# Optimization experiments

Hardware: AMD Instinct MI355X
Metric: run time of the kernel (lower is better)

The kernel has to match this reference:

```python
import jax, jax.numpy as jnp
import numpy as np

B, L1, L2, H = 16, 1024, 1024, 768

def setup_inputs() -> dict:
    key = jax.random.key(0)
    k1, k2, k3, k4, k5, k6 = jax.random.split(key, 6)
    x1 = jax.random.normal(k1, (B, L1, H), dtype=jnp.float32)
    x2 = jax.random.normal(k2, (B, L2, H), dtype=jnp.float32)
    # True = padded position (masked out), matching torch masked_fill_ semantics
    x1_mask = jax.random.randint(k3, (B, L1), 0, 2) == 1
    x2_mask = jax.random.randint(k4, (B, L2), 0, 2) == 1
    # shared nn.Linear(H, H) used for both x and y projections
    W = jax.random.normal(k5, (H, H), dtype=jnp.float32) / np.sqrt(H)
    b = jax.random.normal(k6, (H,), dtype=jnp.float32) * 0.01
    return {"x1": x1, "x2": x2, "x1_mask": x1_mask, "x2_mask": x2_mask, "W": W, "b": b}

def reference(x1, x2, x1_mask, x2_mask, W, b):
    # SeqAttnMatch('relu_FC', normalize='sumY') with z = y = x2
    x_proj = jax.nn.relu(jnp.einsum('bid,hd->bih', x1, W) + b)   # [B,L1,H]
    y_proj = jax.nn.relu(jnp.einsum('bjd,hd->bjh', x2, W) + b)   # [B,L2,H]
    scores = jnp.einsum('bih,bjh->bij', x_proj, y_proj)          # [B,L1,L2]
    scores = jnp.where(x2_mask[:, None, :], -jnp.inf, scores)
    alpha = jax.nn.softmax(scores, axis=-1)                      # sum over len2
    att = jnp.einsum('bij,bjd->bid', alpha, x2)                  # [B,L1,H]
    # inter_att_concat = 'concat_dot_diff'
    return jnp.concatenate([x1, att, x1 * att, x1 - att], axis=2)  # [B,L1,4H]
```

## Files before the change

### kernel.cpp

```cpp
#include <hip/hip_runtime.h>


#define B_  16
#define L_  1024
#define H_  768
#define M1_ (B_ * L_)
#define MT_ (2 * M1_)

using f32x4  = __attribute__((ext_vector_type(4))) float;
using bf16x8 = __attribute__((ext_vector_type(8))) __bf16;
using u16x8  = __attribute__((ext_vector_type(8))) unsigned short;
using u16x4  = __attribute__((ext_vector_type(4))) unsigned short;

__device__ inline unsigned short f2b(float f) {
  unsigned u = __builtin_bit_cast(unsigned, f);
  u += 0x7FFFu + ((u >> 16) & 1u);
  return (unsigned short)(u >> 16);
}
__device__ inline float b2f(unsigned short u) {
  return __builtin_bit_cast(float, ((unsigned)u) << 16);
}

__device__ inline bf16x8 ld_frag(const unsigned short* lds, int row, int quad) {
  u16x8 v = *(const u16x8*)(lds + row * 40 + quad * 8);
  return __builtin_bit_cast(bf16x8, v);
}

#define MFMA(a, b, c) __builtin_amdgcn_mfma_f32_16x16x32_bf16((a), (b), (c), 0, 0, 0)

__global__ __launch_bounds__(256) void k_proj(
    const float* __restrict__ x1, const float* __restrict__ x2,
    const float* __restrict__ W, const float* __restrict__ bias,
    unsigned short* __restrict__ Ph, unsigned short* __restrict__ Pl)
{
  __shared__ unsigned short Ah[128 * 40];
  __shared__ unsigned short Al[128 * 40];
  __shared__ unsigned short Bh[128 * 40];
  __shared__ unsigned short Bl[128 * 40];

  const int tid  = threadIdx.x;
  const int lane = tid & 63, wv = tid >> 6;
  const int wr = wv >> 1, wc = wv & 1;
  const int quad = lane >> 4, lx = lane & 15;

  const int n0 = blockIdx.x * 128;
  const int m0 = blockIdx.y * 128;
  const float* Xb = (m0 < M1_) ? (x1 + (size_t)m0 * H_)
                               : (x2 + (size_t)(m0 - M1_) * H_);

  const int srow = tid >> 1;
  const int scol = (tid & 1) * 16;

  f32x4 acc[4][4] = {};

  for (int k0 = 0; k0 < H_; k0 += 32) {
    __syncthreads();
    const float* sa = Xb + (size_t)srow * H_ + k0 + scol;
    const float* sb = W + (size_t)(n0 + srow) * H_ + k0 + scol;
#pragma unroll
    for (int c = 0; c < 16; c += 4) {
      f32x4 va = *(const f32x4*)(sa + c);
      f32x4 vb = *(const f32x4*)(sb + c);
      u16x4 ha, la, hb, lb;
#pragma unroll
      for (int q = 0; q < 4; ++q) {
        ha[q] = f2b(va[q]); la[q] = f2b(va[q] - b2f(ha[q]));
        hb[q] = f2b(vb[q]); lb[q] = f2b(vb[q] - b2f(hb[q]));
      }
      *(u16x4*)(Ah + srow * 40 + scol + c) = ha;
      *(u16x4*)(Al + srow * 40 + scol + c) = la;
      *(u16x4*)(Bh + srow * 40 + scol + c) = hb;
      *(u16x4*)(Bl + srow * 40 + scol + c) = lb;
    }
    __syncthreads();

    bf16x8 fah[4], fal[4], fbh[4], fbl[4];
#pragma unroll
    for (int t = 0; t < 4; ++t) {
      fah[t] = ld_frag(Ah, wr * 64 + t * 16 + lx, quad);
      fal[t] = ld_frag(Al, wr * 64 + t * 16 + lx, quad);
      fbh[t] = ld_frag(Bh, wc * 64 + t * 16 + lx, quad);
      fbl[t] = ld_frag(Bl, wc * 64 + t * 16 + lx, quad);
    }
#pragma unroll
    for (int i = 0; i < 4; ++i)
#pragma unroll
      for (int j = 0; j < 4; ++j) {
        acc[i][j] = MFMA(fah[i], fbh[j], acc[i][j]);
        acc[i][j] = MFMA(fah[i], fbl[j], acc[i][j]);
        acc[i][j] = MFMA(fal[i], fbh[j], acc[i][j]);
      }
  }

#pragma unroll
  for (int j = 0; j < 4; ++j) {
    const int h = n0 + wc * 64 + j * 16 + lx;
    const float bv = bias[h];
#pragma unroll
    for (int i = 0; i < 4; ++i) {
      const int mb = m0 + wr * 64 + i * 16 + quad * 4;
#pragma unroll
      for (int r = 0; r < 4; ++r) {
        float v = acc[i][j][r] + bv;
        v = v > 0.f ? v : 0.f;
        const unsigned short hh = f2b(v);
        const unsigned short ll = f2b(v - b2f(hh));
        const size_t off = (size_t)(mb + r) * H_ + h;
        Ph[off] = hh;
        Pl[off] = ll;
      }
    }
  }
}

__global__ __launch_bounds__(256) void k_scores(
    const unsigned short* __restrict__ Ph, const unsigned short* __restrict__ Pl,
    const int* __restrict__ x2_mask, float* __restrict__ scores)
{
  __shared__ unsigned short Ah[128 * 40];
  __shared__ unsigned short Al[128 * 40];
  __shared__ unsigned short Bh[128 * 40];
  __shared__ unsigned short Bl[128 * 40];

  const int tid  = threadIdx.x;
  const int lane = tid & 63, wv = tid >> 6;
  const int wr = wv >> 1, wc = wv & 1;
  const int quad = lane >> 4, lx = lane & 15;

  const int j0 = blockIdx.x * 128;
  const int i0 = blockIdx.y * 128;
  const int b  = blockIdx.z;

  const size_t arow = (size_t)(b * L_ + i0);
  const size_t brow = (size_t)(M1_ + b * L_ + j0);

  const int srow = tid >> 1;
  const int scol = (tid & 1) * 16;

  f32x4 acc[4][4] = {};

  for (int k0 = 0; k0 < H_; k0 += 32) {
    __syncthreads();
    const size_t aoff = (arow + srow) * H_ + k0 + scol;
    const size_t boff = (brow + srow) * H_ + k0 + scol;
#pragma unroll
    for (int c = 0; c < 16; c += 8) {
      *(u16x8*)(Ah + srow * 40 + scol + c) = *(const u16x8*)(Ph + aoff + c);
      *(u16x8*)(Al + srow * 40 + scol + c) = *(const u16x8*)(Pl + aoff + c);
      *(u16x8*)(Bh + srow * 40 + scol + c) = *(const u16x8*)(Ph + boff + c);
      *(u16x8*)(Bl + srow * 40 + scol + c) = *(const u16x8*)(Pl + boff + c);
    }
    __syncthreads();

    bf16x8 fah[4], fal[4], fbh[4], fbl[4];
#pragma unroll
    for (int t = 0; t < 4; ++t) {
      fah[t] = ld_frag(Ah, wr * 64 + t * 16 + lx, quad);
      fal[t] = ld_frag(Al, wr * 64 + t * 16 + lx, quad);
      fbh[t] = ld_frag(Bh, wc * 64 + t * 16 + lx, quad);
      fbl[t] = ld_frag(Bl, wc * 64 + t * 16 + lx, quad);
    }
#pragma unroll
    for (int i = 0; i < 4; ++i)
#pragma unroll
      for (int j = 0; j < 4; ++j) {
        acc[i][j] = MFMA(fah[i], fbh[j], acc[i][j]);
        acc[i][j] = MFMA(fah[i], fbl[j], acc[i][j]);
        acc[i][j] = MFMA(fal[i], fbh[j], acc[i][j]);
      }
  }

#pragma unroll
  for (int j = 0; j < 4; ++j) {
    const int jj = j0 + wc * 64 + j * 16 + lx;
    const int mv = x2_mask[b * L_ + jj];
#pragma unroll
    for (int i = 0; i < 4; ++i) {
      const int ib = i0 + wr * 64 + i * 16 + quad * 4;
#pragma unroll
      for (int r = 0; r < 4; ++r) {
        const float v = mv ? -1e30f : acc[i][j][r];
        scores[((size_t)(b * L_) + ib + r) * L_ + jj] = v;
      }
    }
  }
}

__global__ __launch_bounds__(256) void k_softmax(float* __restrict__ scores)
{
  const size_t row = blockIdx.x;
  float* p = scores + row * L_;
  const int tid = threadIdx.x;

  f32x4 v = *(const f32x4*)(p + tid * 4);
  float m = fmaxf(fmaxf(v[0], v[1]), fmaxf(v[2], v[3]));
#pragma unroll
  for (int off = 32; off > 0; off >>= 1) m = fmaxf(m, __shfl_down(m, off));

  __shared__ float rmax[4];
  __shared__ float rsum[4];
  const int wid = tid >> 6, lane = tid & 63;
  if (lane == 0) rmax[wid] = m;
  __syncthreads();
  m = fmaxf(fmaxf(rmax[0], rmax[1]), fmaxf(rmax[2], rmax[3]));

  f32x4 e;
#pragma unroll
  for (int q = 0; q < 4; ++q) e[q] = __expf(v[q] - m);
  float s = e[0] + e[1] + e[2] + e[3];
#pragma unroll
  for (int off = 32; off > 0; off >>= 1) s += __shfl_down(s, off);
  if (lane == 0) rsum[wid] = s;
  __syncthreads();
  s = rsum[0] + rsum[1] + rsum[2] + rsum[3];

  const float inv = 1.0f / s;
#pragma unroll
  for (int q = 0; q < 4; ++q) e[q] *= inv;
  *(f32x4*)(p + tid * 4) = e;
}

__global__ __launch_bounds__(256) void k_att(
    const float* __restrict__ alpha, const float* __restrict__ x2,
    float* __restrict__ att)
{
  __shared__ unsigned short Aa[128 * 40];
  __shared__ unsigned short Bt[128 * 40];

  const int tid  = threadIdx.x;
  const int lane = tid & 63, wv = tid >> 6;
  const int wr = wv >> 1, wc = wv & 1;
  const int quad = lane >> 4, lx = lane & 15;

  const int d0 = blockIdx.x * 128;
  const int i0 = blockIdx.y * 128;
  const int b  = blockIdx.z;

  const int srow = tid >> 1;
  const int scol = (tid & 1) * 16;

  f32x4 acc[4][4] = {};

  for (int j0 = 0; j0 < L_; j0 += 32) {
    __syncthreads();
    const float* sa = alpha + ((size_t)(b * L_) + i0 + srow) * L_ + j0 + scol;
#pragma unroll
    for (int c = 0; c < 16; c += 4) {
      f32x4 va = *(const f32x4*)(sa + c);
      u16x4 h;
#pragma unroll
      for (int q = 0; q < 4; ++q) h[q] = f2b(va[q]);
      *(u16x4*)(Aa + srow * 40 + scol + c) = h;
    }
#pragma unroll
    for (int pp = 0; pp < 4; ++pp) {
      const int idx = tid + pp * 256;
      const int jj  = idx >> 5;
      const int dd  = (idx & 31) * 4;
      f32x4 vb = *(const f32x4*)(x2 + ((size_t)(b * L_) + j0 + jj) * H_ + d0 + dd);
#pragma unroll
      for (int q = 0; q < 4; ++q) Bt[(dd + q) * 40 + jj] = f2b(vb[q]);
    }
    __syncthreads();

    bf16x8 fa[4], fb[4];
#pragma unroll
    for (int t = 0; t < 4; ++t) {
      fa[t] = ld_frag(Aa, wr * 64 + t * 16 + lx, quad);
      fb[t] = ld_frag(Bt, wc * 64 + t * 16 + lx, quad);
    }
#pragma unroll
    for (int i = 0; i < 4; ++i)
#pragma unroll
      for (int j = 0; j < 4; ++j)
        acc[i][j] = MFMA(fa[i], fb[j], acc[i][j]);
  }

#pragma unroll
  for (int j = 0; j < 4; ++j) {
    const int dd = d0 + wc * 64 + j * 16 + lx;
#pragma unroll
    for (int i = 0; i < 4; ++i) {
      const int ib = i0 + wr * 64 + i * 16 + quad * 4;
#pragma unroll
      for (int r = 0; r < 4; ++r)
        att[((size_t)(b * L_) + ib + r) * H_ + dd] = acc[i][j][r];
    }
  }
}

__global__ __launch_bounds__(256) void k_concat(
    const float* __restrict__ x1, const float* __restrict__ att,
    float* __restrict__ out)
{
  const int gid = blockIdx.x * 256 + threadIdx.x;
  const int row = gid / 192;
  const int c   = (gid % 192) * 4;

  f32x4 xv = *(const f32x4*)(x1  + (size_t)row * H_ + c);
  f32x4 av = *(const f32x4*)(att + (size_t)row * H_ + c);
  f32x4 mv, sv;
#pragma unroll
  for (int q = 0; q < 4; ++q) { mv[q] = xv[q] * av[q]; sv[q] = xv[q] - av[q]; }

  float* ob = out + (size_t)row * (4 * H_) + c;
  *(f32x4*)(ob)            = xv;
  *(f32x4*)(ob + H_)       = av;
  *(f32x4*)(ob + 2 * H_)   = mv;
  *(f32x4*)(ob + 3 * H_)   = sv;
}

extern "C" void kernel_launch(void* const* d_in, const int* in_sizes, int n_in,
                              void* d_out, int out_size, void* d_ws, size_t ws_size,
                              hipStream_t stream) {
  const float* x1      = (const float*)d_in[0];
  const float* x2      = (const float*)d_in[1];
  const int*   x2_mask = (const int*)d_in[3];
  const float* W       = (const float*)d_in[4];
  const float* bias    = (const float*)d_in[5];
  float* out = (float*)d_out;

  unsigned short* Ph = (unsigned short*)d_out;
  unsigned short* Pl = (unsigned short*)((char*)d_out + (size_t)MT_ * H_ * 2);
  float* scores      = (float*)((char*)d_out + (size_t)MT_ * H_ * 4);
  float* att         = (float*)d_ws;

  k_proj   <<<dim3(6, 256),   256, 0, stream>>>(x1, x2, W, bias, Ph, Pl);
  k_scores <<<dim3(8, 8, 16), 256, 0, stream>>>(Ph, Pl, x2_mask, scores);
  k_softmax<<<dim3(16384),    256, 0, stream>>>(scores);
  k_att    <<<dim3(6, 8, 16), 256, 0, stream>>>(scores, x2, att);
  k_concat <<<dim3(12288),    256, 0, stream>>>(x1, att, out);
}
```

Before: 720.8 us.

## Pre-split inputs to bf16, use direct global-to-LDS loads with swizzle, bf16 alpha

```diff
diff --git a/kernel.cpp b/kernel.cpp
--- a/kernel.cpp
+++ b/kernel.cpp
@@ -7,6 +7,10 @@
 #define M1_ (B_ * L_)
 #define MT_ (2 * M1_)
 
+#define XB_  24576
+#define WB_  576
+#define TB_  3072
+
 using f32x4  = __attribute__((ext_vector_type(4))) float;
 using bf16x8 = __attribute__((ext_vector_type(8))) __bf16;
 using u16x8  = __attribute__((ext_vector_type(8))) unsigned short;
@@ -21,75 +25,138 @@
   return __builtin_bit_cast(float, ((unsigned)u) << 16);
 }
 
-__device__ inline bf16x8 ld_frag(const unsigned short* lds, int row, int quad) {
-  u16x8 v = *(const u16x8*)(lds + row * 40 + quad * 8);
+__device__ inline void gld16(const void* g, void* l) {
+  __builtin_amdgcn_global_load_lds(
+      (__attribute__((address_space(1))) void*)g,
+      (__attribute__((address_space(3))) void*)l, 16, 0, 0);
+}
+
+__device__ inline bf16x8 ld_frag_sw(const unsigned short* lds, int row, int quad) {
+  const int sl = quad ^ ((row >> 1) & 3);
+  u16x8 v = *(const u16x8*)(lds + row * 32 + sl * 8);
   return __builtin_bit_cast(bf16x8, v);
 }
 
 #define MFMA(a, b, c) __builtin_amdgcn_mfma_f32_16x16x32_bf16((a), (b), (c), 0, 0, 0)
 
+__global__ __launch_bounds__(256) void k_split(
+    const float* __restrict__ x1, const float* __restrict__ x2,
+    const float* __restrict__ W,
+    unsigned short* __restrict__ Xh, unsigned short* __restrict__ Xl,
+    unsigned short* __restrict__ Wh, unsigned short* __restrict__ Wl,
+    unsigned short* __restrict__ x2T)
+{
+  __shared__ unsigned short tile[64][72];
+  const int tid = threadIdx.x;
+  const int bx  = blockIdx.x;
+
+  if (bx < XB_) {
+    const size_t idx = (size_t)bx * 256 + tid;
+    const int row = (int)(idx / 192);
+    const int col = ((int)(idx % 192)) * 4;
+    const float* src = (row < M1_) ? (x1 + (size_t)row * H_ + col)
+                                   : (x2 + (size_t)(row - M1_) * H_ + col);
+    f32x4 v = *(const f32x4*)src;
+    u16x4 h, l;
+#pragma unroll
+    for (int q = 0; q < 4; ++q) { h[q] = f2b(v[q]); l[q] = f2b(v[q] - b2f(h[q])); }
+    *(u16x4*)(Xh + idx * 4) = h;
+    *(u16x4*)(Xl + idx * 4) = l;
+  } else if (bx < XB_ + WB_) {
+    const int idx = (bx - XB_) * 256 + tid;
+    f32x4 v = *(const f32x4*)(W + (size_t)idx * 4);
+    u16x4 h, l;
+#pragma unroll
+    for (int q = 0; q < 4; ++q) { h[q] = f2b(v[q]); l[q] = f2b(v[q] - b2f(h[q])); }
+    *(u16x4*)(Wh + (size_t)idx * 4) = h;
+    *(u16x4*)(Wl + (size_t)idx * 4) = l;
+  } else {
+    const int t  = bx - (XB_ + WB_);
+    const int b  = t / 192;
+    const int r  = t % 192;
+    const int j0 = (r / 12) * 64;
+    const int d0 = (r % 12) * 64;
+#pragma unroll
+    for (int p = 0; p < 4; ++p) {
+      const int idx = tid + p * 256;
+      const int jr  = idx >> 4;
+      const int dc  = (idx & 15) * 4;
+      f32x4 v = *(const f32x4*)(x2 + ((size_t)(b * L_ + j0 + jr)) * H_ + d0 + dc);
+#pragma unroll
+      for (int q = 0; q < 4; ++q) tile[jr][dc + q] = f2b(v[q]);
+    }
+    __syncthreads();
+#pragma unroll
+    for (int p = 0; p < 2; ++p) {
+      const int idx = tid + p * 256;
+      const int dr  = idx >> 3;
+      const int jc  = (idx & 7) * 8;
+      u16x8 o;
+#pragma unroll
+      for (int q = 0; q < 8; ++q) o[q] = tile[jc + q][dr];
+      *(u16x8*)(x2T + ((size_t)(b * H_) + d0 + dr) * L_ + j0 + jc) = o;
+    }
+  }
+}
+
 __global__ __launch_bounds__(256) void k_proj(
-    const float* __restrict__ x1, const float* __restrict__ x2,
-    const float* __restrict__ W, const float* __restrict__ bias,
+    const unsigned short* __restrict__ Xh, const unsigned short* __restrict__ Xl,
+    const unsigned short* __restrict__ Wh, const unsigned short* __restrict__ Wl,
+    const float* __restrict__ bias,
     unsigned short* __restrict__ Ph, unsigned short* __restrict__ Pl)
 {
-  __shared__ unsigned short Ah[128 * 40];
-  __shared__ unsigned short Al[128 * 40];
-  __shared__ unsigned short Bh[128 * 40];
-  __shared__ unsigned short Bl[128 * 40];
+  __shared__ unsigned short Ah[128 * 32];
+  __shared__ unsigned short Al[128 * 32];
+  __shared__ unsigned short Bh[128 * 32];
+  __shared__ unsigned short Bl[128 * 32];
 
   const int tid  = threadIdx.x;
   const int lane = tid & 63, wv = tid >> 6;
   const int wr = wv >> 1, wc = wv & 1;
   const int quad = lane >> 4, lx = lane & 15;
+  const int lr = lane >> 2, ls = lane & 3;
+  const int lsw = ls ^ ((lr >> 1) & 3);
 
   const int n0 = blockIdx.x * 128;
   const int m0 = blockIdx.y * 128;
-  const float* Xb = (m0 < M1_) ? (x1 + (size_t)m0 * H_)
-                               : (x2 + (size_t)(m0 - M1_) * H_);
-
-  const int srow = tid >> 1;
-  const int scol = (tid & 1) * 16;
 
   f32x4 acc[4][4] = {};
 
   for (int k0 = 0; k0 < H_; k0 += 32) {
     __syncthreads();
-    const float* sa = Xb + (size_t)srow * H_ + k0 + scol;
-    const float* sb = W + (size_t)(n0 + srow) * H_ + k0 + scol;
-#pragma unroll
-    for (int c = 0; c < 16; c += 4) {
-      f32x4 va = *(const f32x4*)(sa + c);
-      f32x4 vb = *(const f32x4*)(sb + c);
-      u16x4 ha, la, hb, lb;
-#pragma unroll
-      for (int q = 0; q < 4; ++q) {
-        ha[q] = f2b(va[q]); la[q] = f2b(va[q] - b2f(ha[q]));
-        hb[q] = f2b(vb[q]); lb[q] = f2b(vb[q] - b2f(hb[q]));
-      }
-      *(u16x4*)(Ah + srow * 40 + scol + c) = ha;
-      *(u16x4*)(Al + srow * 40 + scol + c) = la;
-      *(u16x4*)(Bh + srow * 40 + scol + c) = hb;
-      *(u16x4*)(Bl + srow * 40 + scol + c) = lb;
+#pragma unroll
+    for (int g = 0; g < 2; ++g) {
+      const int rowl = wv * 32 + g * 16;
+      const int row  = rowl + lr;
+      const size_t ga = (size_t)(m0 + row) * H_ + k0 + lsw * 8;
+      const size_t gb = (size_t)(n0 + row) * H_ + k0 + lsw * 8;
+      gld16(Xh + ga, &Ah[rowl * 32]);
+      gld16(Xl + ga, &Al[rowl * 32]);
+      gld16(Wh + gb, &Bh[rowl * 32]);
+      gld16(Wl + gb, &Bl[rowl * 32]);
     }
     __syncthreads();
 
     bf16x8 fah[4], fal[4], fbh[4], fbl[4];
 #pragma unroll
     for (int t = 0; t < 4; ++t) {
-      fah[t] = ld_frag(Ah, wr * 64 + t * 16 + lx, quad);
-      fal[t] = ld_frag(Al, wr * 64 + t * 16 + lx, quad);
-      fbh[t] = ld_frag(Bh, wc * 64 + t * 16 + lx, quad);
-      fbl[t] = ld_frag(Bl, wc * 64 + t * 16 + lx, quad);
-    }
-#pragma unroll
-    for (int i = 0; i < 4; ++i)
-#pragma unroll
-      for (int j = 0; j < 4; ++j) {
-        acc[i][j] = MFMA(fah[i], fbh[j], acc[i][j]);
-        acc[i][j] = MFMA(fah[i], fbl[j], acc[i][j]);
-        acc[i][j] = MFMA(fal[i], fbh[j], acc[i][j]);
-      }
+      fah[t] = ld_frag_sw(Ah, wr * 64 + t * 16 + lx, quad);
+      fal[t] = ld_frag_sw(Al, wr * 64 + t * 16 + lx, quad);
+      fbh[t] = ld_frag_sw(Bh, wc * 64 + t * 16 + lx, quad);
+      fbl[t] = ld_frag_sw(Bl, wc * 64 + t * 16 + lx, quad);
+    }
+#pragma unroll
+    for (int i = 0; i < 4; ++i)
+#pragma unroll
+      for (int j = 0; j < 4; ++j) acc[i][j] = MFMA(fah[i], fbh[j], acc[i][j]);
+#pragma unroll
+    for (int i = 0; i < 4; ++i)
+#pragma unroll
+      for (int j = 0; j < 4; ++j) acc[i][j] = MFMA(fah[i], fbl[j], acc[i][j]);
+#pragma unroll
+    for (int i = 0; i < 4; ++i)
+#pragma unroll
+      for (int j = 0; j < 4; ++j) acc[i][j] = MFMA(fal[i], fbh[j], acc[i][j]);
   }
 
 #pragma unroll
@@ -117,57 +184,59 @@
     const unsigned short* __restrict__ Ph, const unsigned short* __restrict__ Pl,
     const int* __restrict__ x2_mask, float* __restrict__ scores)
 {
-  __shared__ unsigned short Ah[128 * 40];
-  __shared__ unsigned short Al[128 * 40];
-  __shared__ unsigned short Bh[128 * 40];
-  __shared__ unsigned short Bl[128 * 40];
+  __shared__ unsigned short Ah[128 * 32];
+  __shared__ unsigned short Al[128 * 32];
+  __shared__ unsigned short Bh[128 * 32];
+  __shared__ unsigned short Bl[128 * 32];
 
   const int tid  = threadIdx.x;
   const int lane = tid & 63, wv = tid >> 6;
   const int wr = wv >> 1, wc = wv & 1;
   const int quad = lane >> 4, lx = lane & 15;
+  const int lr = lane >> 2, ls = lane & 3;
+  const int lsw = ls ^ ((lr >> 1) & 3);
 
   const int j0 = blockIdx.x * 128;
   const int i0 = blockIdx.y * 128;
   const int b  = blockIdx.z;
 
-  const size_t arow = (size_t)(b * L_ + i0);
-  const size_t brow = (size_t)(M1_ + b * L_ + j0);
-
-  const int srow = tid >> 1;
-  const int scol = (tid & 1) * 16;
-
   f32x4 acc[4][4] = {};
 
   for (int k0 = 0; k0 < H_; k0 += 32) {
     __syncthreads();
-    const size_t aoff = (arow + srow) * H_ + k0 + scol;
-    const size_t boff = (brow + srow) * H_ + k0 + scol;
-#pragma unroll
-    for (int c = 0; c < 16; c += 8) {
-      *(u16x8*)(Ah + srow * 40 + scol + c) = *(const u16x8*)(Ph + aoff + c);
-      *(u16x8*)(Al + srow * 40 + scol + c) = *(const u16x8*)(Pl + aoff + c);
-      *(u16x8*)(Bh + srow * 40 + scol + c) = *(const u16x8*)(Ph + boff + c);
-      *(u16x8*)(Bl + srow * 40 + scol + c) = *(const u16x8*)(Pl + boff + c);
+#pragma unroll
+    for (int g = 0; g < 2; ++g) {
+      const int rowl = wv * 32 + g * 16;
+      const int row  = rowl + lr;
+      const size_t ga = (size_t)(b * L_ + i0 + row) * H_ + k0 + lsw * 8;
+      const size_t gb = (size_t)(M1_ + b * L_ + j0 + row) * H_ + k0 + lsw * 8;
+      gld16(Ph + ga, &Ah[rowl * 32]);
+      gld16(Pl + ga, &Al[rowl * 32]);
+      gld16(Ph + gb, &Bh[rowl * 32]);
+      gld16(Pl + gb, &Bl[rowl * 32]);
     }
     __syncthreads();
 
     bf16x8 fah[4], fal[4], fbh[4], fbl[4];
 #pragma unroll
     for (int t = 0; t < 4; ++t) {
-      fah[t] = ld_frag(Ah, wr * 64 + t * 16 + lx, quad);
-      fal[t] = ld_frag(Al, wr * 64 + t * 16 + lx, quad);
-      fbh[t] = ld_frag(Bh, wc * 64 + t * 16 + lx, quad);
-      fbl[t] = ld_frag(Bl, wc * 64 + t * 16 + lx, quad);
-    }
-#pragma unroll
-    for (int i = 0; i < 4; ++i)
-#pragma unroll
-      for (int j = 0; j < 4; ++j) {
-        acc[i][j] = MFMA(fah[i], fbh[j], acc[i][j]);
-        acc[i][j] = MFMA(fah[i], fbl[j], acc[i][j]);
-        acc[i][j] = MFMA(fal[i], fbh[j], acc[i][j]);
-      }
+      fah[t] = ld_frag_sw(Ah, wr * 64 + t * 16 + lx, quad);
+      fal[t] = ld_frag_sw(Al, wr * 64 + t * 16 + lx, quad);
+      fbh[t] = ld_frag_sw(Bh, wc * 64 + t * 16 + lx, quad);
+      fbl[t] = ld_frag_sw(Bl, wc * 64 + t * 16 + lx, quad);
+    }
+#pragma unroll
+    for (int i = 0; i < 4; ++i)
+#pragma unroll
+      for (int j = 0; j < 4; ++j) acc[i][j] = MFMA(fah[i], fbh[j], acc[i][j]);
+#pragma unroll
+    for (int i = 0; i < 4; ++i)
+#pragma unroll
+      for (int j = 0; j < 4; ++j) acc[i][j] = MFMA(fah[i], fbl[j], acc[i][j]);
+#pragma unroll
+    for (int i = 0; i < 4; ++i)
+#pragma unroll
+      for (int j = 0; j < 4; ++j) acc[i][j] = MFMA(fal[i], fbh[j], acc[i][j]);
   }
 
 #pragma unroll
@@ -186,10 +255,11 @@
   }
 }
 
-__global__ __launch_bounds__(256) void k_softmax(float* __restrict__ scores)
+__global__ __launch_bounds__(256) void k_softmax(
+    const float* __restrict__ scores, unsigned short* __restrict__ alphab)
 {
   const size_t row = blockIdx.x;
-  float* p = scores + row * L_;
+  const float* p = scores + row * L_;
   const int tid = threadIdx.x;
 
   f32x4 v = *(const f32x4*)(p + tid * 4);
@@ -215,59 +285,50 @@
   s = rsum[0] + rsum[1] + rsum[2] + rsum[3];
 
   const float inv = 1.0f / s;
-#pragma unroll
-  for (int q = 0; q < 4; ++q) e[q] *= inv;
-  *(f32x4*)(p + tid * 4) = e;
+  u16x4 o;
+#pragma unroll
+  for (int q = 0; q < 4; ++q) o[q] = f2b(e[q] * inv);
+  *(u16x4*)(alphab + row * L_ + tid * 4) = o;
 }
 
 __global__ __launch_bounds__(256) void k_att(
-    const float* __restrict__ alpha, const float* __restrict__ x2,
+    const unsigned short* __restrict__ alphab, const unsigned short* __restrict__ x2T,
     float* __restrict__ att)
 {
-  __shared__ unsigned short Aa[128 * 40];
-  __shared__ unsigned short Bt[128 * 40];
+  __shared__ unsigned short Aa[128 * 32];
+  __shared__ unsigned short Bt[128 * 32];
 
   const int tid  = threadIdx.x;
   const int lane = tid & 63, wv = tid >> 6;
   const int wr = wv >> 1, wc = wv & 1;
   const int quad = lane >> 4, lx = lane & 15;
+  const int lr = lane >> 2, ls = lane & 3;
+  const int lsw = ls ^ ((lr >> 1) & 3);
 
   const int d0 = blockIdx.x * 128;
   const int i0 = blockIdx.y * 128;
   const int b  = blockIdx.z;
 
-  const int srow = tid >> 1;
-  const int scol = (tid & 1) * 16;
-
   f32x4 acc[4][4] = {};
 
   for (int j0 = 0; j0 < L_; j0 += 32) {
     __syncthreads();
-    const float* sa = alpha + ((size_t)(b * L_) + i0 + srow) * L_ + j0 + scol;
-#pragma unroll
-    for (int c = 0; c < 16; c += 4) {
-      f32x4 va = *(const f32x4*)(sa + c);
-      u16x4 h;
-#pragma unroll
-      for (int q = 0; q < 4; ++q) h[q] = f2b(va[q]);
-      *(u16x4*)(Aa + srow * 40 + scol + c) = h;
-    }
-#pragma unroll
-    for (int pp = 0; pp < 4; ++pp) {
-      const int idx = tid + pp * 256;
-      const int jj  = idx >> 5;
-      const int dd  = (idx & 31) * 4;
-      f32x4 vb = *(const f32x4*)(x2 + ((size_t)(b * L_) + j0 + jj) * H_ + d0 + dd);
-#pragma unroll
-      for (int q = 0; q < 4; ++q) Bt[(dd + q) * 40 + jj] = f2b(vb[q]);
+#pragma unroll
+    for (int g = 0; g < 2; ++g) {
+      const int rowl = wv * 32 + g * 16;
+      const int row  = rowl + lr;
+      const size_t ga = (size_t)(b * L_ + i0 + row) * L_ + j0 + lsw * 8;
+      const size_t gb = ((size_t)(b * H_) + d0 + row) * L_ + j0 + lsw * 8;
+      gld16(alphab + ga, &Aa[rowl * 32]);
+      gld16(x2T + gb, &Bt[rowl * 32]);
     }
     __syncthreads();
 
     bf16x8 fa[4], fb[4];
 #pragma unroll
     for (int t = 0; t < 4; ++t) {
-      fa[t] = ld_frag(Aa, wr * 64 + t * 16 + lx, quad);
-      fb[t] = ld_frag(Bt, wc * 64 + t * 16 + lx, quad);
+      fa[t] = ld_frag_sw(Aa, wr * 64 + t * 16 + lx, quad);
+      fb[t] = ld_frag_sw(Bt, wc * 64 + t * 16 + lx, quad);
     }
 #pragma unroll
     for (int i = 0; i < 4; ++i)
@@ -304,10 +365,10 @@
   for (int q = 0; q < 4; ++q) { mv[q] = xv[q] * av[q]; sv[q] = xv[q] - av[q]; }
 
   float* ob = out + (size_t)row * (4 * H_) + c;
-  *(f32x4*)(ob)            = xv;
-  *(f32x4*)(ob + H_)       = av;
-  *(f32x4*)(ob + 2 * H_)   = mv;
-  *(f32x4*)(ob + 3 * H_)   = sv;
+  *(f32x4*)(ob)          = xv;
+  *(f32x4*)(ob + H_)     = av;
+  *(f32x4*)(ob + 2 * H_) = mv;
+  *(f32x4*)(ob + 3 * H_) = sv;
 }
 
 extern "C" void kernel_launch(void* const* d_in, const int* in_sizes, int n_in,
@@ -320,14 +381,22 @@
   const float* bias    = (const float*)d_in[5];
   float* out = (float*)d_out;
 
-  unsigned short* Ph = (unsigned short*)d_out;
-  unsigned short* Pl = (unsigned short*)((char*)d_out + (size_t)MT_ * H_ * 2);
-  float* scores      = (float*)((char*)d_out + (size_t)MT_ * H_ * 4);
-  float* att         = (float*)d_ws;
-
-  k_proj   <<<dim3(6, 256),   256, 0, stream>>>(x1, x2, W, bias, Ph, Pl);
+  char* o8 = (char*)d_out;
+  unsigned short* Ph     = (unsigned short*)o8;
+  unsigned short* Pl     = (unsigned short*)(o8 + 50331648);
+  float*          scores = (float*)(o8 + 100663296);
+  unsigned short* Xh     = (unsigned short*)(o8 + 100663296);
+  unsigned short* Wh     = (unsigned short*)(o8 + 167772160);
+  unsigned short* Wl     = (unsigned short*)(o8 + 168951808);
+  unsigned short* x2T    = (unsigned short*)(o8 + 170131456);
+  unsigned short* alphab = (unsigned short*)o8;
+  unsigned short* Xl     = (unsigned short*)d_ws;
+  float*          att    = (float*)d_ws;
+
+  k_split  <<<dim3(XB_ + WB_ + TB_), 256, 0, stream>>>(x1, x2, W, Xh, Xl, Wh, Wl, x2T);
+  k_proj   <<<dim3(6, 256),   256, 0, stream>>>(Xh, Xl, Wh, Wl, bias, Ph, Pl);
   k_scores <<<dim3(8, 8, 16), 256, 0, stream>>>(Ph, Pl, x2_mask, scores);
-  k_softmax<<<dim3(16384),    256, 0, stream>>>(scores);
-  k_att    <<<dim3(6, 8, 16), 256, 0, stream>>>(scores, x2, att);
+  k_softmax<<<dim3(16384),    256, 0, stream>>>(scores, alphab);
+  k_att    <<<dim3(6, 8, 16), 256, 0, stream>>>(scores ? alphab : alphab, x2T, att);
   k_concat <<<dim3(12288),    256, 0, stream>>>(x1, att, out);
 }
```

Result: faster. 649.3 us (-9.9%).
